# Kernel tuning notes

Measured on AMD Instinct MI355X. Metric: run time of the kernel, lower is better.

Reference implementation:

```python
import jax, jax.numpy as jnp
import numpy as np

B, D, E, H, L = 8, 1024, 256, 8, 2
HD = E // H
NBITS = int(np.floor(np.log2(D))) + 1  # 11
NEG = -1e30  # additive mask value (stands in for -inf, grad-safe)


def _binary_codes():
    codes = np.stack([[int(b) for b in format(i + 1, '0%db' % NBITS)] for i in range(D)]).astype(np.float32) - 0.5
    return jnp.asarray(codes)  # [D, NBITS]


def _alibi():
    idx = np.arange(D, dtype=np.float32)
    dist = np.abs(idx[None, :] - idx[:, None])
    slopes = 2.0 ** (-np.arange(H, dtype=np.float32) / H)
    return jnp.asarray(slopes[:, None, None] * dist[None])  # [H, D, D]


def _layernorm(x, w, b, eps=1e-5):
    m = x.mean(-1, keepdims=True)
    v = ((x - m) ** 2).mean(-1, keepdims=True)
    return (x - m) / jnp.sqrt(v + eps) * w + b


def setup_inputs():
    key = jax.random.key(0)
    ks = jax.random.split(key, 12)
    n = lambda k, s, sc=0.05: jax.random.normal(k, s, jnp.float32) * sc
    return dict(
        x=jax.random.normal(ks[0], (B, D), jnp.float32),
        value_w=n(ks[1], (E,)),
        value_b=jnp.zeros((E,), jnp.float32),
        feature_embed=n(ks[2], (D, E), 0.02),
        binary_w=n(ks[3], (E, NBITS)),
        qw=n(ks[4], (E, E)),
        kw=n(ks[5], (E, E)),
        vw=n(ks[6], (E, E)),
        film_alpha=jnp.asarray(0.1, jnp.float32),
        film_a=jnp.asarray(1.0, jnp.float32),
        ln1_w=jnp.ones((E,), jnp.float32),
        ln1_b=jnp.zeros((E,), jnp.float32),
        ffn_w1=n(ks[7], (2 * E, E)),
        ffn_b1=jnp.zeros((2 * E,), jnp.float32),
        ffn_w2=n(ks[8], (E, 2 * E)),
        ffn_b2=jnp.zeros((E,), jnp.float32),
        gamma_attn=jnp.full((E,), 0.01, jnp.float32),
        gamma_ffn=jnp.full((E,), 0.01, jnp.float32),
        corr_ln_w=jnp.ones((E,), jnp.float32),
        corr_ln_b=jnp.zeros((E,), jnp.float32),
        corr_w1=n(ks[9], (E, E)),
        corr_b1=jnp.zeros((E,), jnp.float32),
        corr_w2=n(ks[10], (1, E)),
        corr_b2=jnp.zeros((1,), jnp.float32),
        alibi_strength=jnp.asarray(0.1, jnp.float32),
    )


def reference(x, value_w, value_b, feature_embed, binary_w, qw, kw, vw,
              film_alpha, film_a, ln1_w, ln1_b, ffn_w1, ffn_b1, ffn_w2, ffn_b2,
              gamma_attn, gamma_ffn, corr_ln_w, corr_ln_b, corr_w1, corr_b1,
              corr_w2, corr_b2, alibi_strength):
    codes = _binary_codes()
    alibi = _alibi()
    eye = jnp.eye(D, dtype=bool)
    mask_add = jnp.where(eye, NEG, 0.0).astype(x.dtype)      # no-self additive mask [D, D]
    allowed = (~eye).astype(x.dtype)                          # allowed_bool after update (all but self)

    pos = feature_embed + codes @ binary_w.T                  # [D, E] positional stream
    Q0 = jnp.broadcast_to(pos, (B, D, E))                     # queries: NO value leakage
    kv = x[..., None] * value_w + value_b + pos               # [B, D, E] keys/values include x

    # FiLM gain from mean of neighbor values (no self)
    deg = jnp.maximum(allowed.sum(axis=1), 1.0)               # [D]
    x_neigh = (x @ allowed) / deg                             # [B, D]
    q_scale = jnp.clip(1.0 + jnp.tanh(film_alpha) * jnp.tanh(film_a * x_neigh), 0.7, 1.3)

    # K/V projections are layer-shared and KV is constant -> hoist out of loop
    k = (kv @ kw.T).reshape(B, D, H, HD).transpose(0, 2, 1, 3)  # [B, H, D, HD]
    v = (kv @ vw.T).reshape(B, D, H, HD).transpose(0, 2, 1, 3)
    strength = jnp.maximum(alibi_strength, 0.0)
    bias = mask_add[None, None] - strength * alibi[None]        # [1, H, D, D]

    h = Q0
    for _ in range(L):
        q = (h @ qw.T).reshape(B, D, H, HD).transpose(0, 2, 1, 3)
        q = q * q_scale[:, None, :, None]
        scores = jnp.einsum('bhqe,bhke->bhqk', q, k) / np.float32(np.sqrt(HD)) + bias
        aw = jax.nn.softmax(scores, axis=-1)                    # dropout off (eval)
        attn = jnp.einsum('bhqk,bhke->bhqe', aw, v)
        attn = attn.transpose(0, 2, 1, 3).reshape(B, D, E)
        h = h + gamma_attn * attn                               # drop_path off (eval)
        y = _layernorm(h, ln1_w, ln1_b)
        y = jax.nn.gelu(y @ ffn_w1.T + ffn_b1, approximate=False)
        y = y @ ffn_w2.T + ffn_b2
        h = h + gamma_ffn * y

    # correction head: LN -> Linear -> GELU -> Linear(->1)
    y = _layernorm(h, corr_ln_w, corr_ln_b)
    y = jax.nn.gelu(y @ corr_w1.T + corr_b1, approximate=False)
    out = (y @ corr_w2.T + corr_b2)[..., 0]                     # [B, D]
    return out
```

## Files before the change

kernel.cpp:

```cpp
#include <hip/hip_runtime.h>
#include <math.h>

#define BD 8
#define DD 1024
#define EE 256
#define HH 8
#define HDD 32
#define NBITS 11

typedef __attribute__((ext_vector_type(8))) short short8;
typedef __attribute__((ext_vector_type(4))) float f4;

__device__ __forceinline__ ushort f2bf(float f) {
  unsigned u = __float_as_uint(f);
  u += 0x7fffu + ((u >> 16) & 1u);
  return (ushort)(u >> 16);
}
__device__ __forceinline__ void async_copy16(ushort* lds, const ushort* g) {
  __builtin_amdgcn_global_load_lds((const __attribute__((address_space(1))) void*)g,
                                   (__attribute__((address_space(3))) void*)lds, 16, 0, 0);
}

__global__ __launch_bounds__(256) void k_pro(const float* __restrict__ x,
                                             const float* __restrict__ value_w,
                                             const float* __restrict__ value_b,
                                             const float* __restrict__ fe,
                                             const float* __restrict__ binary_w,
                                             ushort* __restrict__ kv_bf,
                                             float* __restrict__ h,
                                             const float* __restrict__ film_alpha,
                                             const float* __restrict__ film_a,
                                             float* __restrict__ qscale,
                                             const float* __restrict__ qw,
                                             const float* __restrict__ kw,
                                             const float* __restrict__ vw,
                                             const float* __restrict__ w1,
                                             const float* __restrict__ w2,
                                             const float* __restrict__ cw1,
                                             ushort* __restrict__ o) {
  if (blockIdx.x < 8192) {
    int idx = blockIdx.x * 256 + threadIdx.x;
    int e = idx & (EE - 1);
    int d = (idx >> 8) & (DD - 1);
    int b = idx >> 18;
    float p = fe[d * EE + e];
    int code = d + 1;
    #pragma unroll
    for (int bit = 0; bit < NBITS; bit++) {
      float cb = (float)((code >> (NBITS - 1 - bit)) & 1) - 0.5f;
      p += cb * binary_w[e * NBITS + bit];
    }
    kv_bf[idx] = f2bf(x[b * DD + d] * value_w[e] + value_b[e] + p);
    h[idx] = p;
  } else if (blockIdx.x < 8200) {
    __shared__ float red[256];
    int b = blockIdx.x - 8192, t = threadIdx.x;
    float s = 0.f;
    #pragma unroll
    for (int i = 0; i < 4; i++) s += x[b * DD + t + i * 256];
    red[t] = s; __syncthreads();
    for (int off = 128; off > 0; off >>= 1) {
      if (t < off) red[t] += red[t + off];
      __syncthreads();
    }
    float total = red[0];
    float ta = tanhf(film_alpha[0]);
    float fa = film_a[0];
    #pragma unroll
    for (int i = 0; i < 4; i++) {
      int d = t + i * 256;
      float xn = (total - x[b * DD + d]) / 1023.0f;
      float qs = 1.0f + ta * tanhf(fa * xn);
      qs = fminf(fmaxf(qs, 0.7f), 1.3f);
      qscale[b * DD + d] = qs;
    }
  } else {
    int i = (int)(blockIdx.x - 8200) * 256 + threadIdx.x;
    float v;
    if (i < 65536) v = qw[i];
    else if (i < 131072) v = kw[i - 65536];
    else if (i < 196608) v = vw[i - 131072];
    else if (i < 327680) v = w1[i - 196608];
    else if (i < 458752) v = w2[i - 327680];
    else v = cw1[i - 458752];
    o[i] = f2bf(v);
  }
}

template <int KT>
__global__ __launch_bounds__(512) void kvgemm_k(const ushort* __restrict__ A,
                                                const ushort* __restrict__ Bw,
                                                ushort* __restrict__ C,
                                                ushort* __restrict__ C2) {
  __shared__ ushort As[2][128 * 64];
  __shared__ ushort Bs[2][64 * 64];
  int tid = threadIdx.x;
  int w = tid >> 6, lane = tid & 63;
  int c = lane & 15, g = lane >> 4;
  int wr = w >> 1, wc = w & 1;
  int lr = lane >> 3, lsl = lane & 7;

  const ushort* Ab = A + (size_t)(blockIdx.y * 128) * KT;
  const ushort* Bb = Bw + (size_t)(blockIdx.x * 64) * KT;

  f4 acc[2][2] = {};
  const int NT = KT / 64;

#define STAGE(buf, kt) do {                                                                   \
    _Pragma("unroll")                                                                         \
    for (int j = 0; j < 2; j++) {                                                             \
      int rl = j * 64 + w * 8 + lr;                                                           \
      int slot = lsl ^ (rl & 7);                                                              \
      async_copy16(&As[buf][(j * 64 + w * 8) * 64], Ab + (size_t)rl * KT + (kt) * 64 + slot * 8); \
    }                                                                                         \
    { int rl = w * 8 + lr; int slot = lsl ^ (rl & 7);                                         \
      async_copy16(&Bs[buf][(w * 8) * 64], Bb + (size_t)rl * KT + (kt) * 64 + slot * 8); }    \
  } while (0)

  STAGE(0, 0);
  __syncthreads();

  #pragma unroll
  for (int kt = 0; kt < NT; kt++) {
    int cur = kt & 1;
    if (kt + 1 < NT) STAGE(cur ^ 1, kt + 1);
    #pragma unroll
    for (int ks2 = 0; ks2 < 2; ks2++) {
      short8 af[2], bf_[2];
      #pragma unroll
      for (int mi = 0; mi < 2; mi++) {
        int rowl = wr * 32 + mi * 16 + c;
        int slot = (ks2 * 4 + g) ^ (rowl & 7);
        af[mi] = *(const short8*)&As[cur][rowl * 64 + slot * 8];
      }
      #pragma unroll
      for (int ni = 0; ni < 2; ni++) {
        int rowl = wc * 32 + ni * 16 + c;
        int slot = (ks2 * 4 + g) ^ (rowl & 7);
        bf_[ni] = *(const short8*)&Bs[cur][rowl * 64 + slot * 8];
      }
      #pragma unroll
      for (int mi = 0; mi < 2; mi++)
        #pragma unroll
        for (int ni = 0; ni < 2; ni++)
          acc[mi][ni] = __builtin_amdgcn_mfma_f32_16x16x32_bf16(af[mi], bf_[ni], acc[mi][ni], 0, 0, 0);
    }
    __syncthreads();
  }
#undef STAGE

  int m0 = blockIdx.y * 128 + wr * 32;
  int n0 = blockIdx.x * 64 + wc * 32;
  #pragma unroll
  for (int mi = 0; mi < 2; mi++) {
    #pragma unroll
    for (int ni = 0; ni < 2; ni++) {
      #pragma unroll
      for (int r = 0; r < 4; r++) {
        int row = m0 + mi * 16 + 4 * g + r;
        int col = n0 + ni * 16 + c;
        float v = acc[mi][ni][r];
        int bI = row >> 10, dI = row & 1023;
        if (col < 256) {
          int hI = col >> 5, eI = col & 31;
          C[(((size_t)(bI * HH + hI)) * DD + dI) * HDD + eI] = f2bf(v);
        } else {
          int ch = col - 256;
          int hI = ch >> 5, eI = ch & 31;
          C2[(((size_t)(bI * HH + hI)) * HDD + eI) * DD + dI] = f2bf(v);
        }
      }
    }
  }
}

__global__ __launch_bounds__(512, 2) void mega_k(const float* __restrict__ h0,
                                              const ushort* __restrict__ qwb,
                                              const float* __restrict__ qscale,
                                              const ushort* __restrict__ Kbf,
                                              const ushort* __restrict__ Vtb,
                                              const float* __restrict__ gamma_attn,
                                              const float* __restrict__ strength_p,
                                              const float* __restrict__ lnw,
                                              const float* __restrict__ lnb,
                                              const ushort* __restrict__ w1b,
                                              const float* __restrict__ fb1,
                                              const ushort* __restrict__ w2b,
                                              const float* __restrict__ fb2,
                                              const float* __restrict__ gamma_ffn,
                                              const float* __restrict__ clnw,
                                              const float* __restrict__ clnb,
                                              const ushort* __restrict__ cw1b,
                                              const float* __restrict__ cb1,
                                              const float* __restrict__ cw2,
                                              const float* __restrict__ cb2,
                                              float* __restrict__ out) {
  __shared__ __align__(16) float hs[32][256];
  __shared__ __align__(16) ushort S1[32 * 256];
  __shared__ __align__(16) char Rb[33280];

  ushort (*Pl)[16][88] = (ushort (*)[16][88])Rb;
  float (*upd)[260]    = (float (*)[260])Rb;
  ushort* tt           = (ushort*)Rb;
  float (*red)[32]     = (float (*)[32])Rb;

  int tid = threadIdx.x;
  int w = tid >> 6, lane = tid & 63;
  int c = lane & 15, g = lane >> 4;
  int lid = ((blockIdx.x & 7) << 5) + (blockIdx.x >> 3);
  int b = lid >> 5;
  int chunk = lid & 31;
  int q0 = chunk * 32;
  int hh = w;
  int bh = b * HH + hh;
  int dtile = q0 >> 6;
  float ss = fmaxf(strength_p[0], 0.f) * exp2f(-(float)hh / 8.0f);
  const float L2E = 1.4426950408889634f;

  #pragma unroll
  for (int i = 0; i < 4; i++) {
    int j = tid + i * 512;
    int row = j >> 6;
    int col = (j & 63) * 4;
    const float4 v = *(const float4*)&h0[((size_t)(b * DD + q0 + row)) * EE + col];
    *(float4*)&hs[row][col] = v;
    ushort4 o;
    o.x = f2bf(v.x); o.y = f2bf(v.y); o.z = f2bf(v.z); o.w = f2bf(v.w);
    int sp = (col >> 3) ^ (row & 7);
    *(ushort4*)&S1[row * 256 + sp * 8 + (col & 7)] = o;
  }
  __syncthreads();

  #pragma unroll 1
  for (int layer = 0; layer < 2; layer++) {
    short8 qf[2];
    #pragma unroll
    for (int G = 0; G < 2; G++) {
      f4 qa0 = {0.f, 0.f, 0.f, 0.f}, qa1 = {0.f, 0.f, 0.f, 0.f};
      int rowA = G * 16 + c;
      const ushort* Bb0 = qwb + ((size_t)(hh * HDD + c)) * EE + 8 * g;
      const ushort* Bb1 = Bb0 + (size_t)16 * EE;
      #pragma unroll
      for (int kk = 0; kk < 8; kk++) {
        int sp = (kk * 4 + g) ^ (rowA & 7);
        short8 a  = *(const short8*)&S1[rowA * 256 + sp * 8];
        short8 b0 = *(const short8*)(Bb0 + kk * 32);
        short8 b1 = *(const short8*)(Bb1 + kk * 32);
        qa0 = __builtin_amdgcn_mfma_f32_16x16x32_bf16(a, b0, qa0, 0, 0, 0);
        qa1 = __builtin_amdgcn_mfma_f32_16x16x32_bf16(a, b1, qa1, 0, 0, 0);
      }
      const float4 qsv = *(const float4*)&qscale[b * DD + q0 + G * 16 + 4 * g];
      float qs[4] = {qsv.x, qsv.y, qsv.z, qsv.w};
      #pragma unroll
      for (int r = 0; r < 4; r++) {
        float sc = qs[r] * 0.17677669529663687f;
        Pl[w][4 * g + r][c]      = f2bf(qa0[r] * sc);
        Pl[w][4 * g + r][16 + c] = f2bf(qa1[r] * sc);
      }
      qf[G] = *(const short8*)&Pl[w][c][8 * g];
    }

    int Wi = (ss > 1e-8f) ? (int)fminf(14.0f / ss, 1.0e6f) : 1000000;
    int hi = min(15, (q0 + 31 + Wi) >> 6);
    int tlo = q0 - 63 - Wi;
    int lo = (tlo <= 0) ? 0 : ((tlo + 63) >> 6);

    f4 oacc[2][2] = {};
    float lpart[2] = {0.f, 0.f};
    const ushort* Kb0 = Kbf + (((size_t)bh * DD + c) << 5) + (g << 3);
    const ushort* Vb0 = Vtb + ((size_t)(bh * HDD + c)) * DD + (g << 3);

    #pragma unroll 1
    for (int ks = lo; ks <= hi; ks++) {
      short8 kf[4];
      #pragma unroll
      for (int t = 0; t < 4; t++)
        kf[t] = *(const short8*)(Kb0 + (((size_t)(ks * 64 + t * 16)) << 5));
      const ushort* vb = Vb0 + ks * 64;
      short8 va0 = *(const short8*)(vb);
      short8 va1 = *(const short8*)(vb + 32);
      short8 vc0 = *(const short8*)(vb + (size_t)16 * DD);
      short8 vc1 = *(const short8*)(vb + (size_t)16 * DD + 32);
      float sgn = (ks > dtile) ? -ss : ss;
      #pragma unroll
      for (int G = 0; G < 2; G++) {
        int qg = q0 + G * 16 + c;
        f4 z = {0.f, 0.f, 0.f, 0.f};
        f4 sa[4];
        #pragma unroll
        for (int t = 0; t < 4; t++)
          sa[t] = __builtin_amdgcn_mfma_f32_16x16x32_bf16(kf[t], qf[G], z, 0, 0, 0);
        float s[16];
        if (ks == dtile) {
          #pragma unroll
          for (int t = 0; t < 4; t++) {
            #pragma unroll
            for (int r = 0; r < 4; r++) {
              int k = ks * 64 + t * 16 + 4 * g + r;
              float ad = fabsf((float)(qg - k));
              s[t * 4 + r] = (k == qg) ? -1e30f : fmaf(-ss, ad, sa[t][r]);
            }
          }
        } else {
          int kb2 = ks * 64 + 4 * g - qg;
          #pragma unroll
          for (int t = 0; t < 4; t++) {
            #pragma unroll
            for (int r = 0; r < 4; r++) {
              float dk = (float)(kb2 + t * 16 + r);
              s[t * 4 + r] = fmaf(sgn, dk, sa[t][r]);
            }
          }
        }
        float lp = 0.f;
        #pragma unroll
        for (int i = 0; i < 16; i++) {
          float p = exp2f(s[i] * L2E);
          s[i] = p;
          lp += p;
        }
        lpart[G] += lp;
        #pragma unroll
        for (int t = 0; t < 4; t++) {
          uint2 u;
          u.x = __builtin_amdgcn_perm(__float_as_uint(s[t * 4 + 1]), __float_as_uint(s[t * 4 + 0]), 0x07060302u);
          u.y = __builtin_amdgcn_perm(__float_as_uint(s[t * 4 + 3]), __float_as_uint(s[t * 4 + 2]), 0x07060302u);
          *(uint2*)&Pl[w][c][t * 16 + 4 * g] = u;
        }
        short8 pa0 = *(const short8*)&Pl[w][c][8 * g];
        short8 pa1 = *(const short8*)&Pl[w][c][32 + 8 * g];
        oacc[G][0] = __builtin_amdgcn_mfma_f32_16x16x32_bf16(pa0, va0, oacc[G][0], 0, 0, 0);
        oacc[G][1] = __builtin_amdgcn_mfma_f32_16x16x32_bf16(pa0, vc0, oacc[G][1], 0, 0, 0);
        oacc[G][0] = __builtin_amdgcn_mfma_f32_16x16x32_bf16(pa1, va1, oacc[G][0], 0, 0, 0);
        oacc[G][1] = __builtin_amdgcn_mfma_f32_16x16x32_bf16(pa1, vc1, oacc[G][1], 0, 0, 0);
      }
    }
    float linv[2];
    #pragma unroll
    for (int G = 0; G < 2; G++) {
      lpart[G] += __shfl_xor(lpart[G], 16);
      lpart[G] += __shfl_xor(lpart[G], 32);
      linv[G] = 1.0f / lpart[G];
    }
    __syncthreads();

    #pragma unroll
    for (int G = 0; G < 2; G++) {
      #pragma unroll
      for (int r = 0; r < 4; r++) {
        float li = __shfl(linv[G], 4 * g + r);
        int row = G * 16 + 4 * g + r;
        int e0 = hh * HDD + c, e1 = hh * HDD + 16 + c;
        upd[row][e0] = gamma_attn[e0] * oacc[G][0][r] * li;
        upd[row][e1] = gamma_attn[e1] * oacc[G][1][r] * li;
      }
    }
    __syncthreads();

    #pragma unroll
    for (int rr = 0; rr < 4; rr++) {
      int row = 4 * w + rr;
      const float4 hv = *(const float4*)&hs[row][4 * lane];
      const float4 uv = *(const float4*)&upd[row][4 * lane];
      float4 v;
      v.x = hv.x + uv.x; v.y = hv.y + uv.y; v.z = hv.z + uv.z; v.w = hv.w + uv.w;
      *(float4*)&hs[row][4 * lane] = v;
      float s  = v.x + v.y + v.z + v.w;
      float s2 = v.x * v.x + v.y * v.y + v.z * v.z + v.w * v.w;
      #pragma unroll
      for (int off = 32; off; off >>= 1) {
        s  += __shfl_xor(s, off);
        s2 += __shfl_xor(s2, off);
      }
      float mean = s * (1.0f / EE);
      float var = s2 * (1.0f / EE) - mean * mean;
      float rs = rsqrtf(var + 1e-5f);
      const float4 wv = *(const float4*)&lnw[4 * lane];
      const float4 bv = *(const float4*)&lnb[4 * lane];
      ushort4 o;
      o.x = f2bf((v.x - mean) * rs * wv.x + bv.x);
      o.y = f2bf((v.y - mean) * rs * wv.y + bv.y);
      o.z = f2bf((v.z - mean) * rs * wv.z + bv.z);
      o.w = f2bf((v.w - mean) * rs * wv.w + bv.w);
      int sp = (lane >> 1) ^ (row & 7);
      *(ushort4*)&S1[row * 256 + sp * 8 + (lane & 1) * 4] = o;
    }
    __syncthreads();

    f4 acc2[2][2] = {};
    #pragma unroll 1
    for (int H = 0; H < 2; H++) {
      f4 acc1[2][2] = {};
      #pragma unroll
      for (int kstep = 0; kstep < 8; kstep++) {
        short8 af[2], bf_[2];
        #pragma unroll
        for (int mi = 0; mi < 2; mi++) {
          int row = mi * 16 + c;
          int sp = (kstep * 4 + g) ^ (row & 7);
          af[mi] = *(const short8*)&S1[row * 256 + sp * 8];
        }
        #pragma unroll
        for (int ni = 0; ni < 2; ni++) {
          int col = H * 256 + w * 32 + ni * 16 + c;
          bf_[ni] = *(const short8*)(w1b + (size_t)col * EE + kstep * 32 + 8 * g);
        }
        #pragma unroll
        for (int mi = 0; mi < 2; mi++)
          #pragma unroll
          for (int ni = 0; ni < 2; ni++)
            acc1[mi][ni] = __builtin_amdgcn_mfma_f32_16x16x32_bf16(af[mi], bf_[ni], acc1[mi][ni], 0, 0, 0);
      }
      #pragma unroll
      for (int mi = 0; mi < 2; mi++) {
        #pragma unroll
        for (int ni = 0; ni < 2; ni++) {
          #pragma unroll
          for (int r = 0; r < 4; r++) {
            int row = mi * 16 + 4 * g + r;
            int colH = w * 32 + ni * 16 + c;
            float v = acc1[mi][ni][r] + fb1[H * 256 + colH];
            float gl = 0.5f * v * (1.0f + erff(v * 0.70710678118654752f));
            int sp = (colH >> 3) ^ (row & 7);
            tt[row * 256 + sp * 8 + (colH & 7)] = f2bf(gl);
          }
        }
      }
      __syncthreads();
      #pragma unroll
      for (int kstep = 0; kstep < 8; kstep++) {
        short8 af[2], bf_[2];
        #pragma unroll
        for (int mi = 0; mi < 2; mi++) {
          int row = mi * 16 + c;
          int sp = (kstep * 4 + g) ^ (row & 7);
          af[mi] = *(const short8*)&tt[row * 256 + sp * 8];
        }
        #pragma unroll
        for (int ni = 0; ni < 2; ni++) {
          int col = w * 32 + ni * 16 + c;
          bf_[ni] = *(const short8*)(w2b + (size_t)col * 512 + H * 256 + kstep * 32 + 8 * g);
        }
        #pragma unroll
        for (int mi = 0; mi < 2; mi++)
          #pragma unroll
          for (int ni = 0; ni < 2; ni++)
            acc2[mi][ni] = __builtin_amdgcn_mfma_f32_16x16x32_bf16(af[mi], bf_[ni], acc2[mi][ni], 0, 0, 0);
      }
      __syncthreads();
    }
    #pragma unroll
    for (int mi = 0; mi < 2; mi++) {
      #pragma unroll
      for (int ni = 0; ni < 2; ni++) {
        #pragma unroll
        for (int r = 0; r < 4; r++) {
          int row = mi * 16 + 4 * g + r;
          int col = w * 32 + ni * 16 + c;
          float v = acc2[mi][ni][r] + fb2[col];
          hs[row][col] += gamma_ffn[col] * v;
        }
      }
    }
    __syncthreads();

    if (layer == 0) {
      #pragma unroll
      for (int i = 0; i < 4; i++) {
        int j = tid + i * 512;
        int row = j >> 6;
        int col = (j & 63) * 4;
        const float4 v = *(const float4*)&hs[row][col];
        ushort4 o;
        o.x = f2bf(v.x); o.y = f2bf(v.y); o.z = f2bf(v.z); o.w = f2bf(v.w);
        int sp = (col >> 3) ^ (row & 7);
        *(ushort4*)&S1[row * 256 + sp * 8 + (col & 7)] = o;
      }
      __syncthreads();
    }
  }

  #pragma unroll
  for (int rr = 0; rr < 4; rr++) {
    int row = 4 * w + rr;
    const float4 v = *(const float4*)&hs[row][4 * lane];
    float s  = v.x + v.y + v.z + v.w;
    float s2 = v.x * v.x + v.y * v.y + v.z * v.z + v.w * v.w;
    #pragma unroll
    for (int off = 32; off; off >>= 1) {
      s  += __shfl_xor(s, off);
      s2 += __shfl_xor(s2, off);
    }
    float mean = s * (1.0f / EE);
    float var = s2 * (1.0f / EE) - mean * mean;
    float rs = rsqrtf(var + 1e-5f);
    const float4 wv = *(const float4*)&clnw[4 * lane];
    const float4 bv = *(const float4*)&clnb[4 * lane];
    ushort4 o;
    o.x = f2bf((v.x - mean) * rs * wv.x + bv.x);
    o.y = f2bf((v.y - mean) * rs * wv.y + bv.y);
    o.z = f2bf((v.z - mean) * rs * wv.z + bv.z);
    o.w = f2bf((v.w - mean) * rs * wv.w + bv.w);
    int sp = (lane >> 1) ^ (row & 7);
    *(ushort4*)&S1[row * 256 + sp * 8 + (lane & 1) * 4] = o;
  }
  __syncthreads();

  f4 acc[2][2] = {};
  #pragma unroll
  for (int kstep = 0; kstep < 8; kstep++) {
    short8 af[2], bf_[2];
    #pragma unroll
    for (int mi = 0; mi < 2; mi++) {
      int row = mi * 16 + c;
      int sp = (kstep * 4 + g) ^ (row & 7);
      af[mi] = *(const short8*)&S1[row * 256 + sp * 8];
    }
    #pragma unroll
    for (int ni = 0; ni < 2; ni++) {
      int col = w * 32 + ni * 16 + c;
      bf_[ni] = *(const short8*)(cw1b + (size_t)col * EE + kstep * 32 + 8 * g);
    }
    #pragma unroll
    for (int mi = 0; mi < 2; mi++)
      #pragma unroll
      for (int ni = 0; ni < 2; ni++)
        acc[mi][ni] = __builtin_amdgcn_mfma_f32_16x16x32_bf16(af[mi], bf_[ni], acc[mi][ni], 0, 0, 0);
  }
  float b1v[2], w2v[2];
  #pragma unroll
  for (int ni = 0; ni < 2; ni++) {
    int col = w * 32 + ni * 16 + c;
    b1v[ni] = cb1[col];
    w2v[ni] = cw2[col];
  }
  __syncthreads();
  #pragma unroll
  for (int mi = 0; mi < 2; mi++) {
    #pragma unroll
    for (int r = 0; r < 4; r++) {
      float s = 0.f;
      #pragma unroll
      for (int ni = 0; ni < 2; ni++) {
        float v = acc[mi][ni][r] + b1v[ni];
        float gl = 0.5f * v * (1.0f + erff(v * 0.70710678118654752f));
        s += gl * w2v[ni];
      }
      s += __shfl_xor(s, 1);
      s += __shfl_xor(s, 2);
      s += __shfl_xor(s, 4);
      s += __shfl_xor(s, 8);
      if (c == 0) red[w][mi * 16 + 4 * g + r] = s;
    }
  }
  __syncthreads();
  if (tid < 32) {
    float s = 0.f;
    #pragma unroll
    for (int ww = 0; ww < 8; ww++) s += red[ww][tid];
    out[(b << 10) + q0 + tid] = s + cb2[0];
  }
}

extern "C" void kernel_launch(void* const* d_in, const int* in_sizes, int n_in,
                              void* d_out, int out_size, void* d_ws, size_t ws_size,
                              hipStream_t stream) {
  const float* x            = (const float*)d_in[0];
  const float* value_w      = (const float*)d_in[1];
  const float* value_b      = (const float*)d_in[2];
  const float* feature_embed= (const float*)d_in[3];
  const float* binary_w     = (const float*)d_in[4];
  const float* qw           = (const float*)d_in[5];
  const float* kw           = (const float*)d_in[6];
  const float* vw           = (const float*)d_in[7];
  const float* film_alpha   = (const float*)d_in[8];
  const float* film_a       = (const float*)d_in[9];
  const float* ln1_w        = (const float*)d_in[10];
  const float* ln1_b        = (const float*)d_in[11];
  const float* ffn_w1       = (const float*)d_in[12];
  const float* ffn_b1       = (const float*)d_in[13];
  const float* ffn_w2       = (const float*)d_in[14];
  const float* ffn_b2       = (const float*)d_in[15];
  const float* gamma_attn   = (const float*)d_in[16];
  const float* gamma_ffn    = (const float*)d_in[17];
  const float* corr_ln_w    = (const float*)d_in[18];
  const float* corr_ln_b    = (const float*)d_in[19];
  const float* corr_w1      = (const float*)d_in[20];
  const float* corr_b1      = (const float*)d_in[21];
  const float* corr_w2      = (const float*)d_in[22];
  const float* corr_b2      = (const float*)d_in[23];
  const float* alibi_strength=(const float*)d_in[24];

  const size_t ME = (size_t)BD * DD * EE;
  float* ws = (float*)d_ws;
  float* qscale = ws;
  float* hb     = qscale + BD * DD;
  ushort* kv_bf = (ushort*)(hb + ME);
  ushort* Kbf   = kv_bf + ME;
  ushort* Vtb   = Kbf + ME;
  ushort* wbf   = Vtb + ME;
  ushort* qwb   = wbf;
  ushort* kwb   = wbf + 65536;
  ushort* w1b   = wbf + 196608;
  ushort* w2b   = wbf + 327680;
  ushort* cw1b  = wbf + 458752;

  const int M = BD * DD;

  k_pro<<<8192 + 8 + 2048, 256, 0, stream>>>(x, value_w, value_b, feature_embed, binary_w,
                                             kv_bf, hb,
                                             film_alpha, film_a, qscale,
                                             qw, kw, vw, ffn_w1, ffn_w2, corr_w1, wbf);

  kvgemm_k<256><<<dim3(512 / 64, M / 128), 512, 0, stream>>>(kv_bf, kwb, Kbf, Vtb);

  mega_k<<<dim3(256), 512, 0, stream>>>(hb, qwb, qscale, Kbf, Vtb,
                                        gamma_attn, alibi_strength,
                                        ln1_w, ln1_b,
                                        w1b, ffn_b1, w2b, ffn_b2, gamma_ffn,
                                        corr_ln_w, corr_ln_b,
                                        cw1b, corr_b1, corr_w2, corr_b2,
                                        (float*)d_out);
}
```

Before: 131.7 us.

## Halve query rows per mega_k block to launch 512 blocks with higher occupancy

Each block of the fused attention+FFN kernel now handles 16 query rows instead of 32. The grid doubles to 512 blocks, shared memory per block shrinks, and launch bounds rise to 4 blocks per CU. The aim is to fill all CUs on the MI355X, since 256 blocks underfill them. The cost is that K/V tiles and FFN weights are read twice as often overall, and each loaded weight fragment feeds fewer MFMAs.

Result: slower. 404.1 us, median of 2 (+206.8%).

```diff
diff --git a/kernel.cpp b/kernel.cpp
--- a/kernel.cpp
+++ b/kernel.cpp
@@ -174,7 +174,7 @@
   }
 }
 
-__global__ __launch_bounds__(512, 2) void mega_k(const float* __restrict__ h0,
+__global__ __launch_bounds__(512, 4) void mega_k(const float* __restrict__ h0,
                                               const ushort* __restrict__ qwb,
                                               const float* __restrict__ qscale,
                                               const ushort* __restrict__ Kbf,
@@ -195,30 +195,30 @@
                                               const float* __restrict__ cw2,
                                               const float* __restrict__ cb2,
                                               float* __restrict__ out) {
-  __shared__ __align__(16) float hs[32][256];
-  __shared__ __align__(16) ushort S1[32 * 256];
-  __shared__ __align__(16) char Rb[33280];
+  __shared__ __align__(16) float hs[16][256];
+  __shared__ __align__(16) ushort S1[16 * 256];
+  __shared__ __align__(16) char Rb[22528];
 
   ushort (*Pl)[16][88] = (ushort (*)[16][88])Rb;
   float (*upd)[260]    = (float (*)[260])Rb;
   ushort* tt           = (ushort*)Rb;
-  float (*red)[32]     = (float (*)[32])Rb;
+  float (*red)[16]     = (float (*)[16])Rb;
 
   int tid = threadIdx.x;
   int w = tid >> 6, lane = tid & 63;
   int c = lane & 15, g = lane >> 4;
-  int lid = ((blockIdx.x & 7) << 5) + (blockIdx.x >> 3);
-  int b = lid >> 5;
-  int chunk = lid & 31;
-  int q0 = chunk * 32;
+  int lid = ((blockIdx.x & 7) << 6) + (blockIdx.x >> 3);
+  int b = lid >> 6;
+  int chunk = lid & 63;
+  int q0 = chunk * 16;
   int hh = w;
   int bh = b * HH + hh;
-  int dtile = q0 >> 6;
+  int dtile = chunk >> 2;
   float ss = fmaxf(strength_p[0], 0.f) * exp2f(-(float)hh / 8.0f);
   const float L2E = 1.4426950408889634f;
 
   #pragma unroll
-  for (int i = 0; i < 4; i++) {
+  for (int i = 0; i < 2; i++) {
     int j = tid + i * 512;
     int row = j >> 6;
     int col = (j & 63) * 4;
@@ -233,11 +233,10 @@
 
   #pragma unroll 1
   for (int layer = 0; layer < 2; layer++) {
-    short8 qf[2];
-    #pragma unroll
-    for (int G = 0; G < 2; G++) {
+    short8 qf;
+    {
       f4 qa0 = {0.f, 0.f, 0.f, 0.f}, qa1 = {0.f, 0.f, 0.f, 0.f};
-      int rowA = G * 16 + c;
+      int rowA = c;
       const ushort* Bb0 = qwb + ((size_t)(hh * HDD + c)) * EE + 8 * g;
       const ushort* Bb1 = Bb0 + (size_t)16 * EE;
       #pragma unroll
@@ -249,7 +248,7 @@
         qa0 = __builtin_amdgcn_mfma_f32_16x16x32_bf16(a, b0, qa0, 0, 0, 0);
         qa1 = __builtin_amdgcn_mfma_f32_16x16x32_bf16(a, b1, qa1, 0, 0, 0);
       }
-      const float4 qsv = *(const float4*)&qscale[b * DD + q0 + G * 16 + 4 * g];
+      const float4 qsv = *(const float4*)&qscale[b * DD + q0 + 4 * g];
       float qs[4] = {qsv.x, qsv.y, qsv.z, qsv.w};
       #pragma unroll
       for (int r = 0; r < 4; r++) {
@@ -257,16 +256,18 @@
         Pl[w][4 * g + r][c]      = f2bf(qa0[r] * sc);
         Pl[w][4 * g + r][16 + c] = f2bf(qa1[r] * sc);
       }
-      qf[G] = *(const short8*)&Pl[w][c][8 * g];
+      qf = *(const short8*)&Pl[w][c][8 * g];
     }
 
     int Wi = (ss > 1e-8f) ? (int)fminf(14.0f / ss, 1.0e6f) : 1000000;
-    int hi = min(15, (q0 + 31 + Wi) >> 6);
+    int hi = min(15, (q0 + 15 + Wi) >> 6);
     int tlo = q0 - 63 - Wi;
     int lo = (tlo <= 0) ? 0 : ((tlo + 63) >> 6);
 
-    f4 oacc[2][2] = {};
-    float lpart[2] = {0.f, 0.f};
+    f4 oacc0 = {0.f, 0.f, 0.f, 0.f};
+    f4 oacc1 = {0.f, 0.f, 0.f, 0.f};
+    float lpart = 0.f;
+    int qg = q0 + c;
     const ushort* Kb0 = Kbf + (((size_t)bh * DD + c) << 5) + (g << 3);
     const ushort* Vb0 = Vtb + ((size_t)(bh * HDD + c)) * DD + (g << 3);
 
@@ -281,85 +282,72 @@
       short8 va1 = *(const short8*)(vb + 32);
       short8 vc0 = *(const short8*)(vb + (size_t)16 * DD);
       short8 vc1 = *(const short8*)(vb + (size_t)16 * DD + 32);
-      float sgn = (ks > dtile) ? -ss : ss;
-      #pragma unroll
-      for (int G = 0; G < 2; G++) {
-        int qg = q0 + G * 16 + c;
-        f4 z = {0.f, 0.f, 0.f, 0.f};
-        f4 sa[4];
+      f4 z = {0.f, 0.f, 0.f, 0.f};
+      f4 sa[4];
+      #pragma unroll
+      for (int t = 0; t < 4; t++)
+        sa[t] = __builtin_amdgcn_mfma_f32_16x16x32_bf16(kf[t], qf, z, 0, 0, 0);
+      float s[16];
+      if (ks == dtile) {
         #pragma unroll
-        for (int t = 0; t < 4; t++)
-          sa[t] = __builtin_amdgcn_mfma_f32_16x16x32_bf16(kf[t], qf[G], z, 0, 0, 0);
-        float s[16];
-        if (ks == dtile) {
+        for (int t = 0; t < 4; t++) {
           #pragma unroll
-          for (int t = 0; t < 4; t++) {
-            #pragma unroll
-            for (int r = 0; r < 4; r++) {
-              int k = ks * 64 + t * 16 + 4 * g + r;
-              float ad = fabsf((float)(qg - k));
-              s[t * 4 + r] = (k == qg) ? -1e30f : fmaf(-ss, ad, sa[t][r]);
-            }
-          }
-        } else {
-          int kb2 = ks * 64 + 4 * g - qg;
-          #pragma unroll
-          for (int t = 0; t < 4; t++) {
-            #pragma unroll
-            for (int r = 0; r < 4; r++) {
-              float dk = (float)(kb2 + t * 16 + r);
-              s[t * 4 + r] = fmaf(sgn, dk, sa[t][r]);
-            }
+          for (int r = 0; r < 4; r++) {
+            int k = ks * 64 + t * 16 + 4 * g + r;
+            float ad = fabsf((float)(qg - k));
+            s[t * 4 + r] = (k == qg) ? -1e30f : fmaf(-ss, ad, sa[t][r]);
           }
         }
-        float lp = 0.f;
-        #pragma unroll
-        for (int i = 0; i < 16; i++) {
-          float p = exp2f(s[i] * L2E);
-          s[i] = p;
-          lp += p;
-        }
-        lpart[G] += lp;
+      } else {
+        float sgn = (ks > dtile) ? -ss : ss;
+        int kb2 = ks * 64 + 4 * g - qg;
         #pragma unroll
         for (int t = 0; t < 4; t++) {
-          uint2 u;
-          u.x = __builtin_amdgcn_perm(__float_as_uint(s[t * 4 + 1]), __float_as_uint(s[t * 4 + 0]), 0x07060302u);
-          u.y = __builtin_amdgcn_perm(__float_as_uint(s[t * 4 + 3]), __float_as_uint(s[t * 4 + 2]), 0x07060302u);
-          *(uint2*)&Pl[w][c][t * 16 + 4 * g] = u;
+          #pragma unroll
+          for (int r = 0; r < 4; r++) {
+            float dk = (float)(kb2 + t * 16 + r);
+            s[t * 4 + r] = fmaf(sgn, dk, sa[t][r]);
+          }
         }
-        short8 pa0 = *(const short8*)&Pl[w][c][8 * g];
-        short8 pa1 = *(const short8*)&Pl[w][c][32 + 8 * g];
-        oacc[G][0] = __builtin_amdgcn_mfma_f32_16x16x32_bf16(pa0, va0, oacc[G][0], 0, 0, 0);
-        oacc[G][1] = __builtin_amdgcn_mfma_f32_16x16x32_bf16(pa0, vc0, oacc[G][1], 0, 0, 0);
-        oacc[G][0] = __builtin_amdgcn_mfma_f32_16x16x32_bf16(pa1, va1, oacc[G][0], 0, 0, 0);
-        oacc[G][1] = __builtin_amdgcn_mfma_f32_16x16x32_bf16(pa1, vc1, oacc[G][1], 0, 0, 0);
-      }
-    }
-    float linv[2];
-    #pragma unroll
-    for (int G = 0; G < 2; G++) {
-      lpart[G] += __shfl_xor(lpart[G], 16);
-      lpart[G] += __shfl_xor(lpart[G], 32);
-      linv[G] = 1.0f / lpart[G];
-    }
+      }
+      #pragma unroll
+      for (int i = 0; i < 16; i++) {
+        float p = exp2f(s[i] * L2E);
+        s[i] = p;
+        lpart += p;
+      }
+      #pragma unroll
+      for (int t = 0; t < 4; t++) {
+        uint2 u;
+        u.x = __builtin_amdgcn_perm(__float_as_uint(s[t * 4 + 1]), __float_as_uint(s[t * 4 + 0]), 0x07060302u);
+        u.y = __builtin_amdgcn_perm(__float_as_uint(s[t * 4 + 3]), __float_as_uint(s[t * 4 + 2]), 0x07060302u);
+        *(uint2*)&Pl[w][c][t * 16 + 4 * g] = u;
+      }
+      short8 pa0 = *(const short8*)&Pl[w][c][8 * g];
+      short8 pa1 = *(const short8*)&Pl[w][c][32 + 8 * g];
+      oacc0 = __builtin_amdgcn_mfma_f32_16x16x32_bf16(pa0, va0, oacc0, 0, 0, 0);
+      oacc1 = __builtin_amdgcn_mfma_f32_16x16x32_bf16(pa0, vc0, oacc1, 0, 0, 0);
+      oacc0 = __builtin_amdgcn_mfma_f32_16x16x32_bf16(pa1, va1, oacc0, 0, 0, 0);
+      oacc1 = __builtin_amdgcn_mfma_f32_16x16x32_bf16(pa1, vc1, oacc1, 0, 0, 0);
+    }
+    lpart += __shfl_xor(lpart, 16);
+    lpart += __shfl_xor(lpart, 32);
+    float linv = 1.0f / lpart;
     __syncthreads();
 
     #pragma unroll
-    for (int G = 0; G < 2; G++) {
-      #pragma unroll
-      for (int r = 0; r < 4; r++) {
-        float li = __shfl(linv[G], 4 * g + r);
-        int row = G * 16 + 4 * g + r;
-        int e0 = hh * HDD + c, e1 = hh * HDD + 16 + c;
-        upd[row][e0] = gamma_attn[e0] * oacc[G][0][r] * li;
-        upd[row][e1] = gamma_attn[e1] * oacc[G][1][r] * li;
-      }
+    for (int r = 0; r < 4; r++) {
+      float li = __shfl(linv, 4 * g + r);
+      int row = 4 * g + r;
+      int e0 = hh * HDD + c, e1 = hh * HDD + 16 + c;
+      upd[row][e0] = gamma_attn[e0] * oacc0[r] * li;
+      upd[row][e1] = gamma_attn[e1] * oacc1[r] * li;
     }
     __syncthreads();
 
     #pragma unroll
-    for (int rr = 0; rr < 4; rr++) {
-      int row = 4 * w + rr;
+    for (int rr = 0; rr < 2; rr++) {
+      int row = 2 * w + rr;
       const float4 hv = *(const float4*)&hs[row][4 * lane];
       const float4 uv = *(const float4*)&upd[row][4 * lane];
       float4 v;
@@ -387,86 +375,64 @@
     }
     __syncthreads();
 
-    f4 acc2[2][2] = {};
+    f4 acc2[2] = {};
     #pragma unroll 1
     for (int H = 0; H < 2; H++) {
-      f4 acc1[2][2] = {};
+      f4 acc1[2] = {};
       #pragma unroll
       for (int kstep = 0; kstep < 8; kstep++) {
-        short8 af[2], bf_[2];
-        #pragma unroll
-        for (int mi = 0; mi < 2; mi++) {
-          int row = mi * 16 + c;
-          int sp = (kstep * 4 + g) ^ (row & 7);
-          af[mi] = *(const short8*)&S1[row * 256 + sp * 8];
-        }
+        int row = c;
+        int sp = (kstep * 4 + g) ^ (row & 7);
+        short8 af = *(const short8*)&S1[row * 256 + sp * 8];
         #pragma unroll
         for (int ni = 0; ni < 2; ni++) {
           int col = H * 256 + w * 32 + ni * 16 + c;
-          bf_[ni] = *(const short8*)(w1b + (size_t)col * EE + kstep * 32 + 8 * g);
+          short8 bf_ = *(const short8*)(w1b + (size_t)col * EE + kstep * 32 + 8 * g);
+          acc1[ni] = __builtin_amdgcn_mfma_f32_16x16x32_bf16(af, bf_, acc1[ni], 0, 0, 0);
         }
+      }
+      #pragma unroll
+      for (int ni = 0; ni < 2; ni++) {
         #pragma unroll
-        for (int mi = 0; mi < 2; mi++)
-          #pragma unroll
-          for (int ni = 0; ni < 2; ni++)
-            acc1[mi][ni] = __builtin_amdgcn_mfma_f32_16x16x32_bf16(af[mi], bf_[ni], acc1[mi][ni], 0, 0, 0);
-      }
-      #pragma unroll
-      for (int mi = 0; mi < 2; mi++) {
-        #pragma unroll
-        for (int ni = 0; ni < 2; ni++) {
-          #pragma unroll
-          for (int r = 0; r < 4; r++) {
-            int row = mi * 16 + 4 * g + r;
-            int colH = w * 32 + ni * 16 + c;
-            float v = acc1[mi][ni][r] + fb1[H * 256 + colH];
-            float gl = 0.5f * v * (1.0f + erff(v * 0.70710678118654752f));
-            int sp = (colH >> 3) ^ (row & 7);
-            tt[row * 256 + sp * 8 + (colH & 7)] = f2bf(gl);
-          }
+        for (int r = 0; r < 4; r++) {
+          int row = 4 * g + r;
+          int colH = w * 32 + ni * 16 + c;
+          float v = acc1[ni][r] + fb1[H * 256 + colH];
+          float gl = 0.5f * v * (1.0f + erff(v * 0.70710678118654752f));
+          int sp = (colH >> 3) ^ (row & 7);
+          tt[row * 256 + sp * 8 + (colH & 7)] = f2bf(gl);
         }
       }
       __syncthreads();
       #pragma unroll
       for (int kstep = 0; kstep < 8; kstep++) {
-        short8 af[2], bf_[2];
-        #pragma unroll
-        for (int mi = 0; mi < 2; mi++) {
-          int row = mi * 16 + c;
-          int sp = (kstep * 4 + g) ^ (row & 7);
-          af[mi] = *(const short8*)&tt[row * 256 + sp * 8];
-        }
+        int row = c;
+        int sp = (kstep * 4 + g) ^ (row & 7);
+        short8 af = *(const short8*)&tt[row * 256 + sp * 8];
         #pragma unroll
         for (int ni = 0; ni < 2; ni++) {
           int col = w * 32 + ni * 16 + c;
-          bf_[ni] = *(const short8*)(w2b + (size_t)col * 512 + H * 256 + kstep * 32 + 8 * g);
+          short8 bf_ = *(const short8*)(w2b + (size_t)col * 512 + H * 256 + kstep * 32 + 8 * g);
+          acc2[ni] = __builtin_amdgcn_mfma_f32_16x16x32_bf16(af, bf_, acc2[ni], 0, 0, 0);
         }
-        #pragma unroll
-        for (int mi = 0; mi < 2; mi++)
-          #pragma unroll
-          for (int ni = 0; ni < 2; ni++)
-            acc2[mi][ni] = __builtin_amdgcn_mfma_f32_16x16x32_bf16(af[mi], bf_[ni], acc2[mi][ni], 0, 0, 0);
       }
       __syncthreads();
     }
     #pragma unroll
-    for (int mi = 0; mi < 2; mi++) {
-      #pragma unroll
-      for (int ni = 0; ni < 2; ni++) {
-        #pragma unroll
-        for (int r = 0; r < 4; r++) {
-          int row = mi * 16 + 4 * g + r;
-          int col = w * 32 + ni * 16 + c;
-          float v = acc2[mi][ni][r] + fb2[col];
-          hs[row][col] += gamma_ffn[col] * v;
-        }
+    for (int ni = 0; ni < 2; ni++) {
+      #pragma unroll
+      for (int r = 0; r < 4; r++) {
+        int row = 4 * g + r;
+        int col = w * 32 + ni * 16 + c;
+        float v = acc2[ni][r] + fb2[col];
+        hs[row][col] += gamma_ffn[col] * v;
       }
     }
     __syncthreads();
 
     if (layer == 0) {
       #pragma unroll
-      for (int i = 0; i < 4; i++) {
+      for (int i = 0; i < 2; i++) {
         int j = tid + i * 512;
         int row = j >> 6;
         int col = (j & 63) * 4;
@@ -481,8 +447,8 @@
   }
 
   #pragma unroll
-  for (int rr = 0; rr < 4; rr++) {
-    int row = 4 * w + rr;
+  for (int rr = 0; rr < 2; rr++) {
+    int row = 2 * w + rr;
     const float4 v = *(const float4*)&hs[row][4 * lane];
     float s  = v.x + v.y + v.z + v.w;
     float s2 = v.x * v.x + v.y * v.y + v.z * v.z + v.w * v.w;
@@ -506,26 +472,18 @@
   }
   __syncthreads();
 
-  f4 acc[2][2] = {};
+  f4 acc[2] = {};
   #pragma unroll
   for (int kstep = 0; kstep < 8; kstep++) {
-    short8 af[2], bf_[2];
-    #pragma unroll
-    for (int mi = 0; mi < 2; mi++) {
-      int row = mi * 16 + c;
-      int sp = (kstep * 4 + g) ^ (row & 7);
-      af[mi] = *(const short8*)&S1[row * 256 + sp * 8];
-    }
+    int row = c;
+    int sp = (kstep * 4 + g) ^ (row & 7);
+    short8 af = *(const short8*)&S1[row * 256 + sp * 8];
     #pragma unroll
     for (int ni = 0; ni < 2; ni++) {
       int col = w * 32 + ni * 16 + c;
-      bf_[ni] = *(const short8*)(cw1b + (size_t)col * EE + kstep * 32 + 8 * g);
-    }
-    #pragma unroll
-    for (int mi = 0; mi < 2; mi++)
-      #pragma unroll
-      for (int ni = 0; ni < 2; ni++)
-        acc[mi][ni] = __builtin_amdgcn_mfma_f32_16x16x32_bf16(af[mi], bf_[ni], acc[mi][ni], 0, 0, 0);
+      short8 bf_ = *(const short8*)(cw1b + (size_t)col * EE + kstep * 32 + 8 * g);
+      acc[ni] = __builtin_amdgcn_mfma_f32_16x16x32_bf16(af, bf_, acc[ni], 0, 0, 0);
+    }
   }
   float b1v[2], w2v[2];
   #pragma unroll
@@ -536,25 +494,22 @@
   }
   __syncthreads();
   #pragma unroll
-  for (int mi = 0; mi < 2; mi++) {
-    #pragma unroll
-    for (int r = 0; r < 4; r++) {
-      float s = 0.f;
-      #pragma unroll
-      for (int ni = 0; ni < 2; ni++) {
-        float v = acc[mi][ni][r] + b1v[ni];
-        float gl = 0.5f * v * (1.0f + erff(v * 0.70710678118654752f));
-        s += gl * w2v[ni];
-      }
-      s += __shfl_xor(s, 1);
-      s += __shfl_xor(s, 2);
-      s += __shfl_xor(s, 4);
-      s += __shfl_xor(s, 8);
-      if (c == 0) red[w][mi * 16 + 4 * g + r] = s;
-    }
+  for (int r = 0; r < 4; r++) {
+    float s = 0.f;
+    #pragma unroll
+    for (int ni = 0; ni < 2; ni++) {
+      float v = acc[ni][r] + b1v[ni];
+      float gl = 0.5f * v * (1.0f + erff(v * 0.70710678118654752f));
+      s += gl * w2v[ni];
+    }
+    s += __shfl_xor(s, 1);
+    s += __shfl_xor(s, 2);
+    s += __shfl_xor(s, 4);
+    s += __shfl_xor(s, 8);
+    if (c == 0) red[w][4 * g + r] = s;
   }
   __syncthreads();
-  if (tid < 32) {
+  if (tid < 16) {
     float s = 0.f;
     #pragma unroll
     for (int ww = 0; ww < 8; ww++) s += red[ww][tid];
@@ -614,7 +569,7 @@
 
   kvgemm_k<256><<<dim3(512 / 64, M / 128), 512, 0, stream>>>(kv_bf, kwb, Kbf, Vtb);
 
-  mega_k<<<dim3(256), 512, 0, stream>>>(hb, qwb, qscale, Kbf, Vtb,
+  mega_k<<<dim3(512), 512, 0, stream>>>(hb, qwb, qscale, Kbf, Vtb,
                                         gamma_attn, alibi_strength,
                                         ln1_w, ln1_b,
                                         w1b, ffn_b1, w2b, ffn_b2, gamma_ffn,
```
